# Optimization experiments

Hardware: AMD Instinct MI355X
Metric: run time of the kernel (lower is better)

The kernel has to match this reference:

```python
import jax, jax.numpy as jnp
import numpy as np

N, F_IN, HEADS, F_OUT = 4096, 128, 4, 32
DENSITY = 0.05


def setup_inputs() -> dict:
    key = jax.random.key(0)
    k_x, k_adj, k_w, k_as, k_ad, k_b = jax.random.split(key, 6)
    x = jax.random.normal(k_x, (N, F_IN), dtype=jnp.float32)
    # binary adjacency with self-loops so every row of Tau_sum is nonzero
    adj = (jax.random.uniform(k_adj, (N, N)) < DENSITY).astype(jnp.float32)
    adj = jnp.maximum(adj, jnp.eye(N, dtype=jnp.float32))
    weight = jax.random.normal(k_w, (HEADS * F_OUT, F_IN), dtype=jnp.float32) * 0.1
    att_src = jax.random.normal(k_as, (1, HEADS, F_OUT), dtype=jnp.float32) * 0.1
    att_dst = jax.random.normal(k_ad, (1, HEADS, F_OUT), dtype=jnp.float32) * 0.1
    bias = jax.random.normal(k_b, (HEADS * F_OUT,), dtype=jnp.float32) * 0.1
    return {"x": x, "adj_matrix": adj, "weight": weight,
            "att_src": att_src, "att_dst": att_dst, "bias": bias}


def reference(x, adj_matrix, weight, att_src, att_dst, bias):
    n = x.shape[0]
    heads = att_src.shape[1]
    f_out = weight.shape[0] // heads
    # H' = x W^T, reshaped to [N, heads, F_out]
    h_prime = (x @ weight.T).reshape(n, heads, f_out)
    alpha_src = jnp.sum(h_prime * att_src, axis=-1)  # [N, heads]
    alpha_dst = jnp.sum(h_prime * att_dst, axis=-1)  # [N, heads]
    # C[m, n, h] = alpha_src[n, h] + alpha_dst[m, h]
    C = alpha_src[None, :, :] + alpha_dst[:, None, :]
    adj_t = adj_matrix.T[..., None]                  # [N, N, 1]
    # exp(leaky_relu(C, 0.2)) masked by adjacency
    tau = adj_t * jnp.exp(jnp.maximum(0.2 * C, C))   # [N, N, heads]
    tau_sum = jnp.sum(tau, axis=1, keepdims=True)    # [N, 1, heads]
    att_weights = tau / tau_sum
    # Z[m, h, f] = sum_n (adjT * att)[m, n, h] * H'[n, h, f]
    z = jnp.einsum('mnh,nhf->mhf', adj_t * att_weights, h_prime)
    return z.reshape(n, heads * f_out) + bias
```

## Files before the change

### kernel.cpp

```cpp
#include <hip/hip_runtime.h>
#include <hip/hip_bf16.h>

#define N_NODES 4096
#define F_IN    128
#define HEADS   4
#define FTOT    128
#define NSPLIT  8
#define NRANGE  (N_NODES / NSPLIT)
#define NSTEP   (NRANGE / 64)
#define HPB     512
#define BITB    1024
#define L2E     1.4426950408889634f

typedef __attribute__((ext_vector_type(8)))  short  short8v;
typedef __attribute__((ext_vector_type(16))) float  float16v;

static __device__ __forceinline__ unsigned f2bfu(float f) {
    union { __hip_bfloat16 h; unsigned short u; } cv;
    cv.h = __float2bfloat16(f);
    return (unsigned)cv.u;
}
static __device__ __forceinline__ unsigned cvt_pk_bf16(float lo, float hi) {
    unsigned r;
    asm("v_cvt_pk_bf16_f32 %0, %1, %2" : "=v"(r) : "v"(lo), "v"(hi));
    return r;
}

__global__ __launch_bounds__(256)
void k_pre(const float* __restrict__ x, const float* __restrict__ W,
           const float* __restrict__ att_src, const float* __restrict__ att_dst,
           const float* __restrict__ adj,
           unsigned short* __restrict__ hpt, float* __restrict__ ast,
           float* __restrict__ adt, unsigned* __restrict__ abits)
{
    const int t = threadIdx.x;
    if (blockIdx.x < HPB) {
        __shared__ alignas(16) float    xs[8 * F_IN];
        __shared__ alignas(16) unsigned hs[F_IN * 4];
        __shared__ float ssa[4][8], ssd[4][8];
        const int sub = t >> 7;
        const int tt  = t & 127;
        const int i0  = blockIdx.x * 8;
        reinterpret_cast<float4*>(xs)[t] =
            reinterpret_cast<const float4*>(x + (size_t)i0 * F_IN)[t];
        __syncthreads();

        const float4* W4  = reinterpret_cast<const float4*>(W + tt * F_IN);
        const float4* xs4 = reinterpret_cast<const float4*>(xs + sub * 4 * F_IN);
        float a0 = 0.f, a1 = 0.f, a2 = 0.f, a3 = 0.f;
#pragma unroll
        for (int k = 0; k < F_IN / 4; ++k) {
            const float4 w  = W4[k];
            const float4 v0 = xs4[k], v1 = xs4[32 + k], v2 = xs4[64 + k], v3 = xs4[96 + k];
            a0 = fmaf(w.x, v0.x, a0); a0 = fmaf(w.y, v0.y, a0); a0 = fmaf(w.z, v0.z, a0); a0 = fmaf(w.w, v0.w, a0);
            a1 = fmaf(w.x, v1.x, a1); a1 = fmaf(w.y, v1.y, a1); a1 = fmaf(w.z, v1.z, a1); a1 = fmaf(w.w, v1.w, a1);
            a2 = fmaf(w.x, v2.x, a2); a2 = fmaf(w.y, v2.y, a2); a2 = fmaf(w.z, v2.z, a2); a2 = fmaf(w.w, v2.w, a2);
            a3 = fmaf(w.x, v3.x, a3); a3 = fmaf(w.y, v3.y, a3); a3 = fmaf(w.z, v3.z, a3); a3 = fmaf(w.w, v3.w, a3);
        }
        hs[tt * 4 + sub * 2 + 0] = f2bfu(a0) | (f2bfu(a1) << 16);
        hs[tt * 4 + sub * 2 + 1] = f2bfu(a2) | (f2bfu(a3) << 16);

        const float asv = att_src[tt], adv = att_dst[tt];
        float s0 = a0 * asv, s1 = a1 * asv, s2 = a2 * asv, s3 = a3 * asv;
        float d0 = a0 * adv, d1 = a1 * adv, d2 = a2 * adv, d3 = a3 * adv;
#pragma unroll
        for (int s = 16; s; s >>= 1) {
            s0 += __shfl_xor(s0, s); s1 += __shfl_xor(s1, s);
            s2 += __shfl_xor(s2, s); s3 += __shfl_xor(s3, s);
            d0 += __shfl_xor(d0, s); d1 += __shfl_xor(d1, s);
            d2 += __shfl_xor(d2, s); d3 += __shfl_xor(d3, s);
        }
        if ((tt & 31) == 0) {
            const int hh = tt >> 5;
            ssa[hh][sub * 4 + 0] = s0 * L2E; ssa[hh][sub * 4 + 1] = s1 * L2E;
            ssa[hh][sub * 4 + 2] = s2 * L2E; ssa[hh][sub * 4 + 3] = s3 * L2E;
            ssd[hh][sub * 4 + 0] = d0 * L2E; ssd[hh][sub * 4 + 1] = d1 * L2E;
            ssd[hh][sub * 4 + 2] = d2 * L2E; ssd[hh][sub * 4 + 3] = d3 * L2E;
        }
        __syncthreads();
        if (t < 128)
            *reinterpret_cast<uint4*>(hpt + (size_t)t * N_NODES + i0) =
                *reinterpret_cast<const uint4*>(&hs[t * 4]);
        if (t < 64) {
            const int sd = t >> 5, hh = (t >> 3) & 3, nn = t & 7;
            const float v = sd ? ssd[hh][nn] : ssa[hh][nn];
            (sd ? adt : ast)[hh * N_NODES + i0 + nn] = v;
        }
    } else {
        __shared__ alignas(16) unsigned short lb[64 * 16];
        const int sblk  = blockIdx.x - HPB;
        const int strip = sblk & 63;
        const int chunk = sblk >> 6;
        const int c0    = strip * 64;
        const int r0    = chunk * 256;
        const int q     = t & 15;
        const int p     = t >> 4;
        const float4* adj4 = reinterpret_cast<const float4*>(adj);

        float4 v[16];
#pragma unroll
        for (int it = 0; it < 16; ++it)
            v[it] = adj4[(size_t)(r0 + p * 16 + it) * (N_NODES / 4) + (c0 >> 2) + q];
        unsigned mk0 = 0, mk1 = 0, mk2 = 0, mk3 = 0;
#pragma unroll
        for (int it = 0; it < 16; ++it) {
            mk0 |= (v[it].x != 0.f) ? (1u << it) : 0u;
            mk1 |= (v[it].y != 0.f) ? (1u << it) : 0u;
            mk2 |= (v[it].z != 0.f) ? (1u << it) : 0u;
            mk3 |= (v[it].w != 0.f) ? (1u << it) : 0u;
        }
        lb[(4 * q + 0) * 16 + p] = (unsigned short)mk0;
        lb[(4 * q + 1) * 16 + p] = (unsigned short)mk1;
        lb[(4 * q + 2) * 16 + p] = (unsigned short)mk2;
        lb[(4 * q + 3) * 16 + p] = (unsigned short)mk3;
        __syncthreads();
        const unsigned* lb32 = reinterpret_cast<const unsigned*>(lb);
#pragma unroll
        for (int j = 0; j < 2; ++j) {
            const int w = t + j * 256;
            const int m = w >> 3, col = w & 7;
            abits[(size_t)(c0 + m) * (N_NODES / 32) + chunk * 8 + col] = lb32[w];
        }
    }
}

__global__ __launch_bounds__(256, 4)
void k_main(const unsigned short* __restrict__ hpt, const float* __restrict__ ast,
            const float* __restrict__ adt, const unsigned* __restrict__ abits,
            float* __restrict__ z_part, float* __restrict__ taup)
{
    __shared__ alignas(16) float2 ea_s[HEADS * NRANGE];
    const int t     = threadIdx.x;
    const int wv    = t >> 6;
    const int l     = t & 63;
    const int np    = l >> 5;
    const int lm    = l & 31;
    const int mt    = blockIdx.x >> 3;
    const int split = blockIdx.x & 7;
    const int m0    = mt * 32;
    const int nb0   = split * NRANGE;

#pragma unroll
    for (int j = 0; j < 8; ++j) {
        const int lin = j * 256 + t;
        const int h   = lin >> 9;
        const int n   = lin & 511;
        const float a = ast[h * N_NODES + nb0 + n];
        ea_s[lin] = make_float2(__builtin_amdgcn_exp2f(a),
                                __builtin_amdgcn_exp2f(0.2f * a));
    }
    uint4 brow[4];
    {
        const uint4* bsrc = reinterpret_cast<const uint4*>(
            abits + (size_t)(m0 + lm) * (N_NODES / 32) + split * 16);
#pragma unroll
        for (int j = 0; j < 4; ++j) brow[j] = bsrc[j];
    }
    const float adm = adt[wv * N_NODES + m0 + lm];
    const float ed1 = __builtin_amdgcn_exp2f(adm);
    const float ed2 = __builtin_amdgcn_exp2f(0.2f * adm);
    __syncthreads();

    const unsigned short* hrow = hpt + (size_t)(wv * 32 + lm) * N_NODES + nb0 + np * 8;
    const float2* eaw = ea_s + wv * NRANGE;

    float16v acc, acct;
#pragma unroll
    for (int r = 0; r < 16; ++r) { acc[r] = 0.f; acct[r] = 0.f; }
    union { short8v v; unsigned u[4]; } ones;
#pragma unroll
    for (int j = 0; j < 4; ++j) ones.u[j] = 0x3F803F80u;

    short8v cur[4], nxt[4];
#pragma unroll
    for (int q = 0; q < 4; ++q)
        cur[q] = *reinterpret_cast<const short8v*>(hrow + q * 16);

#pragma unroll
    for (int step = 0; step < NSTEP; ++step) {
        if (step + 1 < NSTEP) {
#pragma unroll
            for (int q = 0; q < 4; ++q)
                nxt[q] = *reinterpret_cast<const short8v*>(hrow + (step + 1) * 64 + q * 16);
        }
#pragma unroll
        for (int q = 0; q < 4; ++q) {
            const float2* eap = eaw + step * 64 + q * 16 + np * 8;
            const unsigned w32 = (&brow[0].x)[((2 * step + (q >> 1)) & 15)];
            const unsigned bb  = (w32 >> (((q & 1) << 4) + (np << 3))) & 0xFFu;
            float w[8];
#pragma unroll
            for (int i = 0; i < 8; ++i) {
                const float2 e = eap[i];
                const float p1 = e.x * ed1;
                const float p2 = e.y * ed2;
                const float sel = (p1 > 1.0f) ? p1 : p2;
                w[i] = (bb & (1u << i)) ? sel : 0.f;
            }
            union { short8v v; unsigned u[4]; } af;
            af.u[0] = cvt_pk_bf16(w[0], w[1]);
            af.u[1] = cvt_pk_bf16(w[2], w[3]);
            af.u[2] = cvt_pk_bf16(w[4], w[5]);
            af.u[3] = cvt_pk_bf16(w[6], w[7]);
            acc  = __builtin_amdgcn_mfma_f32_32x32x16_bf16(af.v, cur[q], acc, 0, 0, 0);
            acct = __builtin_amdgcn_mfma_f32_32x32x16_bf16(af.v, ones.v, acct, 0, 0, 0);
        }
#pragma unroll
        for (int q = 0; q < 4; ++q) cur[q] = nxt[q];
    }

    if (lm == 0) {
#pragma unroll
        for (int r = 0; r < 16; ++r) {
            const int row = (r & 3) + 8 * (r >> 2) + 4 * np;
            taup[((size_t)split * HEADS + wv) * N_NODES + m0 + row] = acct[r];
        }
    }
    float* zp = z_part + (size_t)split * N_NODES * FTOT;
#pragma unroll
    for (int r = 0; r < 16; ++r) {
        const int row = (r & 3) + 8 * (r >> 2) + 4 * np;
        zp[(size_t)(m0 + row) * FTOT + wv * 32 + lm] = acc[r];
    }
}

__global__ __launch_bounds__(256)
void k_fin(const float* __restrict__ z_part, const float* __restrict__ taup,
           const float* __restrict__ bias, float* __restrict__ out)
{
    const int idx = blockIdx.x * 256 + threadIdx.x;
    const int m = idx >> 5, f4 = idx & 31, h = f4 >> 3;
    const float4* zp4 = reinterpret_cast<const float4*>(z_part);
    float4 z = make_float4(0.f, 0.f, 0.f, 0.f);
    float ts = 0.f;
#pragma unroll
    for (int s = 0; s < NSPLIT; ++s) {
        const float4 zs = zp4[(size_t)s * N_NODES * (FTOT / 4) + idx];
        z.x += zs.x; z.y += zs.y; z.z += zs.z; z.w += zs.w;
        ts += taup[((size_t)s * HEADS + h) * N_NODES + m];
    }
    const float inv = 1.f / ts;
    const float4 b = reinterpret_cast<const float4*>(bias)[f4];
    float4 o;
    o.x = z.x * inv + b.x; o.y = z.y * inv + b.y;
    o.z = z.z * inv + b.z; o.w = z.w * inv + b.w;
    reinterpret_cast<float4*>(out)[idx] = o;
}

extern "C" void kernel_launch(void* const* d_in, const int* in_sizes, int n_in,
                              void* d_out, int out_size, void* d_ws, size_t ws_size,
                              hipStream_t stream) {
    const float* x       = (const float*)d_in[0];
    const float* adj     = (const float*)d_in[1];
    const float* weight  = (const float*)d_in[2];
    const float* att_src = (const float*)d_in[3];
    const float* att_dst = (const float*)d_in[4];
    const float* bias    = (const float*)d_in[5];
    float* out = (float*)d_out;

    unsigned short* hpt = (unsigned short*)d_ws;
    float* ast = (float*)(hpt + (size_t)FTOT * N_NODES);
    float* adt = ast + (size_t)HEADS * N_NODES;
    unsigned* abits = (unsigned*)(adt + (size_t)HEADS * N_NODES);
    float* z_part = (float*)(abits + (size_t)N_NODES * (N_NODES / 32));
    float* taup = z_part + (size_t)NSPLIT * N_NODES * FTOT;

    k_pre <<<HPB + BITB, 256, 0, stream>>>(x, weight, att_src, att_dst, adj,
                                           hpt, ast, adt, abits);
    k_main<<<(N_NODES / 32) * NSPLIT, 256, 0, stream>>>(hpt, ast, adt, abits,
                                                        z_part, taup);
    k_fin <<<N_NODES * (FTOT / 4) / 256, 256, 0, stream>>>(z_part, taup, bias, out);
}
```

Before: 47.18 us.

## Double N-splits, store bf16 partials, compute tau sums with VALU instead of MFMA

Raises the N-dimension split from 8 to 16 and occupancy hint to 8 blocks per CU, giving twice as many blocks with half the work each. The second MFMA against a ones vector that computed row sums is replaced with scalar float adds plus a cross-half shuffle, and the leaky-relu select becomes an fmaxf. Partial Z results are stored as bf16 to halve the partial-sum traffic read back by the finalize kernel. The software prefetch of B operands is dropped. Risks: more reduction passes in k_fin, bf16 rounding of partials, and less latency hiding from the removed prefetch.

```diff
diff --git a/kernel.cpp b/kernel.cpp
--- a/kernel.cpp
+++ b/kernel.cpp
@@ -5,7 +5,7 @@
 #define F_IN    128
 #define HEADS   4
 #define FTOT    128
-#define NSPLIT  8
+#define NSPLIT  16
 #define NRANGE  (N_NODES / NSPLIT)
 #define NSTEP   (NRANGE / 64)
 #define HPB     512
@@ -124,10 +124,10 @@
     }
 }
 
-__global__ __launch_bounds__(256, 4)
+__global__ __launch_bounds__(256, 8)
 void k_main(const unsigned short* __restrict__ hpt, const float* __restrict__ ast,
             const float* __restrict__ adt, const unsigned* __restrict__ abits,
-            float* __restrict__ z_part, float* __restrict__ taup)
+            unsigned short* __restrict__ zp16, float* __restrict__ taup)
 {
     __shared__ alignas(16) float2 ea_s[HEADS * NRANGE];
     const int t     = threadIdx.x;
@@ -135,26 +135,26 @@
     const int l     = t & 63;
     const int np    = l >> 5;
     const int lm    = l & 31;
-    const int mt    = blockIdx.x >> 3;
-    const int split = blockIdx.x & 7;
+    const int mt    = blockIdx.x >> 4;
+    const int split = blockIdx.x & 15;
     const int m0    = mt * 32;
     const int nb0   = split * NRANGE;
 
 #pragma unroll
-    for (int j = 0; j < 8; ++j) {
+    for (int j = 0; j < 4; ++j) {
         const int lin = j * 256 + t;
-        const int h   = lin >> 9;
-        const int n   = lin & 511;
+        const int h   = lin >> 8;
+        const int n   = lin & 255;
         const float a = ast[h * N_NODES + nb0 + n];
         ea_s[lin] = make_float2(__builtin_amdgcn_exp2f(a),
                                 __builtin_amdgcn_exp2f(0.2f * a));
     }
-    uint4 brow[4];
+    uint4 brow[2];
     {
         const uint4* bsrc = reinterpret_cast<const uint4*>(
-            abits + (size_t)(m0 + lm) * (N_NODES / 32) + split * 16);
-#pragma unroll
-        for (int j = 0; j < 4; ++j) brow[j] = bsrc[j];
+            abits + (size_t)(m0 + lm) * (N_NODES / 32) + split * 8);
+        brow[0] = bsrc[0];
+        brow[1] = bsrc[1];
     }
     const float adm = adt[wv * N_NODES + m0 + lm];
     const float ed1 = __builtin_amdgcn_exp2f(adm);
@@ -164,79 +164,64 @@
     const unsigned short* hrow = hpt + (size_t)(wv * 32 + lm) * N_NODES + nb0 + np * 8;
     const float2* eaw = ea_s + wv * NRANGE;
 
-    float16v acc, acct;
-#pragma unroll
-    for (int r = 0; r < 16; ++r) { acc[r] = 0.f; acct[r] = 0.f; }
-    union { short8v v; unsigned u[4]; } ones;
-#pragma unroll
-    for (int j = 0; j < 4; ++j) ones.u[j] = 0x3F803F80u;
-
-    short8v cur[4], nxt[4];
-#pragma unroll
-    for (int q = 0; q < 4; ++q)
-        cur[q] = *reinterpret_cast<const short8v*>(hrow + q * 16);
+    float16v acc;
+#pragma unroll
+    for (int r = 0; r < 16; ++r) acc[r] = 0.f;
+    float tau = 0.f;
 
 #pragma unroll
     for (int step = 0; step < NSTEP; ++step) {
-        if (step + 1 < NSTEP) {
-#pragma unroll
-            for (int q = 0; q < 4; ++q)
-                nxt[q] = *reinterpret_cast<const short8v*>(hrow + (step + 1) * 64 + q * 16);
-        }
 #pragma unroll
         for (int q = 0; q < 4; ++q) {
+            const short8v bv = *reinterpret_cast<const short8v*>(hrow + step * 64 + q * 16);
             const float2* eap = eaw + step * 64 + q * 16 + np * 8;
-            const unsigned w32 = (&brow[0].x)[((2 * step + (q >> 1)) & 15)];
+            const unsigned w32 = (&brow[0].x)[(step * 2 + (q >> 1)) & 7];
             const unsigned bb  = (w32 >> (((q & 1) << 4) + (np << 3))) & 0xFFu;
             float w[8];
 #pragma unroll
             for (int i = 0; i < 8; ++i) {
                 const float2 e = eap[i];
-                const float p1 = e.x * ed1;
-                const float p2 = e.y * ed2;
-                const float sel = (p1 > 1.0f) ? p1 : p2;
+                const float sel = fmaxf(e.x * ed1, e.y * ed2);
                 w[i] = (bb & (1u << i)) ? sel : 0.f;
             }
+            const float t01 = w[0] + w[1], t23 = w[2] + w[3];
+            const float t45 = w[4] + w[5], t67 = w[6] + w[7];
+            tau += (t01 + t23) + (t45 + t67);
             union { short8v v; unsigned u[4]; } af;
             af.u[0] = cvt_pk_bf16(w[0], w[1]);
             af.u[1] = cvt_pk_bf16(w[2], w[3]);
             af.u[2] = cvt_pk_bf16(w[4], w[5]);
             af.u[3] = cvt_pk_bf16(w[6], w[7]);
-            acc  = __builtin_amdgcn_mfma_f32_32x32x16_bf16(af.v, cur[q], acc, 0, 0, 0);
-            acct = __builtin_amdgcn_mfma_f32_32x32x16_bf16(af.v, ones.v, acct, 0, 0, 0);
-        }
-#pragma unroll
-        for (int q = 0; q < 4; ++q) cur[q] = nxt[q];
-    }
-
-    if (lm == 0) {
-#pragma unroll
-        for (int r = 0; r < 16; ++r) {
-            const int row = (r & 3) + 8 * (r >> 2) + 4 * np;
-            taup[((size_t)split * HEADS + wv) * N_NODES + m0 + row] = acct[r];
-        }
-    }
-    float* zp = z_part + (size_t)split * N_NODES * FTOT;
+            acc = __builtin_amdgcn_mfma_f32_32x32x16_bf16(af.v, bv, acc, 0, 0, 0);
+        }
+    }
+
+    tau += __shfl_xor(tau, 32);
+    if (np == 0)
+        taup[((size_t)split * HEADS + wv) * N_NODES + m0 + lm] = tau;
+    unsigned short* zp = zp16 + (size_t)split * N_NODES * FTOT;
 #pragma unroll
     for (int r = 0; r < 16; ++r) {
         const int row = (r & 3) + 8 * (r >> 2) + 4 * np;
-        zp[(size_t)(m0 + row) * FTOT + wv * 32 + lm] = acc[r];
+        zp[(size_t)(m0 + row) * FTOT + wv * 32 + lm] = (unsigned short)f2bfu(acc[r]);
     }
 }
 
 __global__ __launch_bounds__(256)
-void k_fin(const float* __restrict__ z_part, const float* __restrict__ taup,
+void k_fin(const unsigned* __restrict__ zp32, const float* __restrict__ taup,
            const float* __restrict__ bias, float* __restrict__ out)
 {
     const int idx = blockIdx.x * 256 + threadIdx.x;
     const int m = idx >> 5, f4 = idx & 31, h = f4 >> 3;
-    const float4* zp4 = reinterpret_cast<const float4*>(z_part);
     float4 z = make_float4(0.f, 0.f, 0.f, 0.f);
     float ts = 0.f;
 #pragma unroll
     for (int s = 0; s < NSPLIT; ++s) {
-        const float4 zs = zp4[(size_t)s * N_NODES * (FTOT / 4) + idx];
-        z.x += zs.x; z.y += zs.y; z.z += zs.z; z.w += zs.w;
+        const uint2 u = reinterpret_cast<const uint2*>(zp32)[(size_t)s * (N_NODES * FTOT / 4) + idx];
+        z.x += __uint_as_float(u.x << 16);
+        z.y += __uint_as_float(u.x & 0xffff0000u);
+        z.z += __uint_as_float(u.y << 16);
+        z.w += __uint_as_float(u.y & 0xffff0000u);
         ts += taup[((size_t)s * HEADS + h) * N_NODES + m];
     }
     const float inv = 1.f / ts;
@@ -262,12 +247,13 @@
     float* ast = (float*)(hpt + (size_t)FTOT * N_NODES);
     float* adt = ast + (size_t)HEADS * N_NODES;
     unsigned* abits = (unsigned*)(adt + (size_t)HEADS * N_NODES);
-    float* z_part = (float*)(abits + (size_t)N_NODES * (N_NODES / 32));
-    float* taup = z_part + (size_t)NSPLIT * N_NODES * FTOT;
+    unsigned short* zp16 = (unsigned short*)(abits + (size_t)N_NODES * (N_NODES / 32));
+    float* taup = (float*)(zp16 + (size_t)NSPLIT * N_NODES * FTOT);
 
     k_pre <<<HPB + BITB, 256, 0, stream>>>(x, weight, att_src, att_dst, adj,
                                            hpt, ast, adt, abits);
     k_main<<<(N_NODES / 32) * NSPLIT, 256, 0, stream>>>(hpt, ast, adt, abits,
-                                                        z_part, taup);
-    k_fin <<<N_NODES * (FTOT / 4) / 256, 256, 0, stream>>>(z_part, taup, bias, out);
-}
+                                                        zp16, taup);
+    k_fin <<<N_NODES * (FTOT / 4) / 256, 256, 0, stream>>>((const unsigned*)zp16,
+                                                           taup, bias, out);
+}
```

Measured after the change: 50.11 us. +6.2%, slower.
